# Performance work log

Hardware: AMD Instinct MI355X
Metric: run time of the kernel (lower is better)

## Reference

```python
import jax, jax.numpy as jnp
import numpy as np

NEG = -9e15  # matches torch's -9000000000000000.0 masking constant


def setup_inputs() -> dict:
    key = jax.random.key(0)
    kq, kk, kv, ka = jax.random.split(key, 4)
    B, H, N, d = 8, 8, 1024, 128
    queries = jax.random.normal(kq, (B, H, N, d), dtype=jnp.float32)
    keys = jax.random.normal(kk, (B, H, N, d), dtype=jnp.float32)
    values = jax.random.normal(kv, (B, H, N, d), dtype=jnp.float32)
    adj = jax.random.randint(ka, (N, N), 0, 2, dtype=jnp.int32)
    return {"queries": queries, "keys": keys, "values": values, "adj": adj}


def reference(queries, keys, values, adj):
    # scores: [B,H,N,N]; original divides by the constant 8 (not sqrt(dim))
    e = jnp.einsum("bhnd,bhmd->bhnm", queries, keys) / 8.0
    # adjacency mask [N,N] broadcasts over batch and heads
    att = jnp.where(adj > 0, e, jnp.asarray(NEG, e.dtype))
    att = jax.nn.softmax(att, axis=-1)
    # dropout is identity in eval mode
    h = jnp.einsum("bhnm,bhmd->bhnd", att, values)  # [B,H,N,d]
    B, H, N, d = h.shape
    # original uses .view (raw reshape), NOT a permute
    return jnp.reshape(h, (N, B, H, d))
```

## Files before the change

kernel.cpp:

```cpp
#include <hip/hip_runtime.h>
#include <hip/hip_bf16.h>


typedef __bf16 bf16x8 __attribute__((ext_vector_type(8)));
typedef float  f32x4  __attribute__((ext_vector_type(4)));
typedef unsigned int u32;
typedef unsigned long long u64;

#define NSEQ 1024
#define DH   128
#define BN   64
#define NKT  16
#define TILE_ELEMS (BN * DH)
#define C1 0.1803368801111244f
#define C2 11.5415603271110070f

__device__ __forceinline__ float f4get(const float4& v, int c) {
    return (c == 0) ? v.x : (c == 1) ? v.y : (c == 2) ? v.z : v.w;
}

__device__ __forceinline__ void gload_lds16(const void* g, void* l) {
    __builtin_amdgcn_global_load_lds(
        (const __attribute__((address_space(1))) u32*)g,
        (__attribute__((address_space(3))) u32*)l, 16, 0, 0);
}

__global__ __launch_bounds__(256)
void prepack_kernel(const float* __restrict__ K, const float* __restrict__ V,
                    __bf16* __restrict__ Kws, __bf16* __restrict__ Vws,
                    u64* __restrict__ adjp, const int* __restrict__ adj)
{
    const int tid = threadIdx.x;
    const int id  = blockIdx.x;

    if (id >= 1024) {
        const int r = (id - 1024) * 16 + (tid >> 4);
        const int c = tid & 15;
        const int* row = adj + (size_t)r * NSEQ + c;
        u64 w = 0;
        #pragma unroll
        for (int j = 0; j < 64; ++j)
            w |= (u64)(row[j * 16] > 0) << j;
        adjp[(size_t)r * 16 + c] = w;
        return;
    }

    const size_t gbase = (size_t)(id >> 4) * NSEQ * DH + (size_t)(id & 15) * BN * DH;
    __bf16* ko = Kws + (size_t)id * TILE_ELEMS;
    __bf16* vo = Vws + (size_t)id * TILE_ELEMS;

    {
        const int r  = tid >> 2;
        const int c0 = (tid & 3) * 4;
        #pragma unroll
        for (int cc = 0; cc < 4; ++cc) {
            const int c = c0 + cc;
            const float* src = K + gbase + (size_t)r * DH + c * 8;
            float4 a = *(const float4*)src;
            float4 b = *(const float4*)(src + 4);
            bf16x8 w;
            w[0]=(__bf16)a.x; w[1]=(__bf16)a.y; w[2]=(__bf16)a.z; w[3]=(__bf16)a.w;
            w[4]=(__bf16)b.x; w[5]=(__bf16)b.y; w[6]=(__bf16)b.z; w[7]=(__bf16)b.w;
            const int cs = (c & 8) | ((c ^ (r & 7)) & 7);
            *(bf16x8*)(ko + r * DH + cs * 8) = w;
        }
    }
    {
        const int vkvb = tid >> 5;
        const int vdb  = tid & 31;
        float4 vr[8];
        #pragma unroll
        for (int rr = 0; rr < 8; ++rr)
            vr[rr] = *(const float4*)(V + gbase + (size_t)(vkvb * 8 + rr) * DH + vdb * 4);
        #pragma unroll
        for (int c = 0; c < 4; ++c) {
            const int d = vdb * 4 + c;
            bf16x8 w;
            #pragma unroll
            for (int j = 0; j < 8; ++j) w[j] = (__bf16)f4get(vr[j], c);
            const int cs = vkvb ^ (d & 7);
            *(bf16x8*)(vo + d * BN + cs * 8) = w;
        }
    }
}

__global__ __launch_bounds__(512, 4)
void attn_fast(const float* __restrict__ Q, const __bf16* __restrict__ Kws,
               const __bf16* __restrict__ Vws, const u64* __restrict__ adjp,
               float* __restrict__ out)
{
    __shared__ __attribute__((aligned(16))) __bf16 Kt[2][TILE_ELEMS];
    __shared__ __attribute__((aligned(16))) __bf16 Vt[TILE_ELEMS];
    __shared__ __attribute__((aligned(16))) __bf16 Ps[128 * 72];

    const int tid  = threadIdx.x;
    const int wave = tid >> 6;
    const int lane = tid & 63;
    const int n16  = lane & 15;
    const int quad = lane >> 4;
    const int m7   = n16 & 7;

    const int id = blockIdx.x;
    const int bh = (id & 7) * 8 + ((id >> 3) & 7);
    const int q0 = (id >> 6) * 128;
    const size_t base  = (size_t)bh * NSEQ * DH;
    const size_t tile0 = (size_t)(bh * NKT) * TILE_ELEMS;
    const int qrb = q0 + wave * 16 + quad * 4;

    bf16x8 qf[4];
    #pragma unroll
    for (int ks = 0; ks < 4; ++ks) {
        const float* src = Q + base + (size_t)(q0 + wave * 16 + n16) * DH
                         + ks * 32 + quad * 8;
        float4 a = *(const float4*)src;
        float4 b = *(const float4*)(src + 4);
        bf16x8 w;
        w[0]=(__bf16)a.x; w[1]=(__bf16)a.y; w[2]=(__bf16)a.z; w[3]=(__bf16)a.w;
        w[4]=(__bf16)b.x; w[5]=(__bf16)b.y; w[6]=(__bf16)b.z; w[7]=(__bf16)b.w;
        qf[ks] = w;
    }

    u64 aw[4];
    #pragma unroll
    for (int i = 0; i < 4; ++i)
        aw[i] = adjp[(size_t)(qrb + i) * 16 + n16];

    f32x4 o[8];
    #pragma unroll
    for (int i = 0; i < 8; ++i) o[i] = (f32x4){0.f, 0.f, 0.f, 0.f};
    float lp[4] = {0.f, 0.f, 0.f, 0.f};

    #pragma unroll
    for (int j = 0; j < 2; ++j) {
        const int off = wave * 1024 + j * 512;
        gload_lds16(Kws + tile0 + off + lane * 8, &Kt[0][off]);
    }

    for (int kt = 0; kt < NKT; ++kt) {
        __builtin_amdgcn_sched_barrier(0);
        asm volatile("s_waitcnt vmcnt(0)" ::: "memory");
        __builtin_amdgcn_sched_barrier(0);
        __builtin_amdgcn_s_barrier();
        __builtin_amdgcn_sched_barrier(0);

        {
            const __bf16* vtile = Vws + tile0 + (size_t)kt * TILE_ELEMS;
            #pragma unroll
            for (int j = 0; j < 2; ++j) {
                const int off = wave * 1024 + j * 512;
                gload_lds16(vtile + off + lane * 8, &Vt[off]);
            }
        }
        __builtin_amdgcn_sched_barrier(0);

        {
            const int ktn = (kt + 1) & (NKT - 1);
            const __bf16* ktile = Kws + tile0 + (size_t)ktn * TILE_ELEMS;
            __bf16* kdst = &Kt[ktn & 1][0];
            #pragma unroll
            for (int j = 0; j < 2; ++j) {
                const int off = wave * 1024 + j * 512;
                gload_lds16(ktile + off + lane * 8, kdst + off);
            }
        }
        __builtin_amdgcn_sched_barrier(0);

        const __bf16* Kc = &Kt[kt & 1][0];
        float sc[4][4];
        __builtin_amdgcn_s_setprio(1);
        #pragma unroll
        for (int t = 0; t < 4; ++t) {
            f32x4 acc = (f32x4){0.f, 0.f, 0.f, 0.f};
            #pragma unroll
            for (int ks = 0; ks < 4; ++ks) {
                const int c  = ks * 4 + quad;
                const int cs = (c & 8) | ((c ^ m7) & 7);
                bf16x8 bfr = *(const bf16x8*)(Kc + (t * 16 + n16) * DH + cs * 8);
                acc = __builtin_amdgcn_mfma_f32_16x16x32_bf16(qf[ks], bfr, acc, 0, 0, 0);
            }
            #pragma unroll
            for (int i = 0; i < 4; ++i) sc[t][i] = acc[i];
        }
        __builtin_amdgcn_s_setprio(0);

        #pragma unroll
        for (int i = 0; i < 4; ++i) {
            const unsigned w4 = (unsigned)(aw[i] >> (kt * 4)) & 0xFu;
            const int prow = wave * 16 + quad * 4 + i;
            float rowsum = 0.f;
            #pragma unroll
            for (int t = 0; t < 4; ++t) {
                float p = exp2f(sc[t][i] * C1 - C2);
                p = (w4 & (1u << t)) ? p : 0.f;
                rowsum += p;
                Ps[prow * 72 + t * 16 + n16] = (__bf16)p;
            }
            lp[i] += rowsum;
        }

        __builtin_amdgcn_sched_barrier(0);
        asm volatile("s_waitcnt vmcnt(2) lgkmcnt(0)" ::: "memory");
        __builtin_amdgcn_sched_barrier(0);
        __builtin_amdgcn_s_barrier();
        __builtin_amdgcn_sched_barrier(0);

        __builtin_amdgcn_s_setprio(1);
        #pragma unroll
        for (int ks = 0; ks < 2; ++ks) {
            bf16x8 pf = *(const bf16x8*)(&Ps[(wave * 16 + n16) * 72 + ks * 32 + quad * 8]);
            #pragma unroll
            for (int nt = 0; nt < 8; ++nt) {
                const int d  = nt * 16 + n16;
                const int cs = (ks * 4 + quad) ^ m7;
                bf16x8 vf = *(const bf16x8*)(&Vt[d * BN + cs * 8]);
                o[nt] = __builtin_amdgcn_mfma_f32_16x16x32_bf16(pf, vf, o[nt], 0, 0, 0);
            }
        }
        __builtin_amdgcn_s_setprio(0);
    }

    float linv[4];
    #pragma unroll
    for (int i = 0; i < 4; ++i) {
        float ls = lp[i];
        ls += __shfl_xor(ls, 1);
        ls += __shfl_xor(ls, 2);
        ls += __shfl_xor(ls, 4);
        ls += __shfl_xor(ls, 8);
        linv[i] = 1.0f / fmaxf(ls, 1e-30f);
    }
    #pragma unroll
    for (int nt = 0; nt < 8; ++nt)
        #pragma unroll
        for (int i = 0; i < 4; ++i)
            out[base + (size_t)(qrb + i) * DH + nt * 16 + n16] = o[nt][i] * linv[i];
}

#define KS_STRIDE 136
#define VT_STRIDE 64
#define PS_STRIDE 72

__global__ __launch_bounds__(256, 4)
void attn_fallback(const float* __restrict__ Q, const float* __restrict__ K,
                   const float* __restrict__ V, const int* __restrict__ adj,
                   float* __restrict__ out)
{
    __shared__ __attribute__((aligned(16))) __bf16 KsP[BN * KS_STRIDE];
    __shared__ __attribute__((aligned(16))) __bf16 Vts[DH * VT_STRIDE];
    const int tid = threadIdx.x;
    const int wave = tid >> 6, lane = tid & 63, n16 = lane & 15, quad = lane >> 4;
    const int id = blockIdx.x;
    const int bh = (id & 7) * 8 + ((id >> 3) & 7);
    const int q0 = (id >> 6) * 64;
    const size_t base = (size_t)bh * NSEQ * DH;
    const int rp = tid >> 4, kcol = (tid & 15) * 8, db = tid & 31, kvb = tid >> 5;
    bf16x8 qf[4];
    #pragma unroll
    for (int ks = 0; ks < 4; ++ks) {
        const float* src = Q + base + (size_t)(q0 + wave * 16 + n16) * DH + ks * 32 + quad * 8;
        float4 a = *(const float4*)src; float4 b = *(const float4*)(src + 4);
        bf16x8 w;
        w[0]=(__bf16)a.x; w[1]=(__bf16)a.y; w[2]=(__bf16)a.z; w[3]=(__bf16)a.w;
        w[4]=(__bf16)b.x; w[5]=(__bf16)b.y; w[6]=(__bf16)b.z; w[7]=(__bf16)b.w;
        qf[ks] = w;
    }
    f32x4 o[8];
    #pragma unroll
    for (int i = 0; i < 8; ++i) o[i] = (f32x4){0.f, 0.f, 0.f, 0.f};
    float lp[4] = {0.f, 0.f, 0.f, 0.f};
    const int qrow = q0 + wave * 16 + quad * 4;
    for (int kt = 0; kt < NKT; ++kt) {
        const int kv0 = kt * BN;
        __syncthreads();
        #pragma unroll
        for (int it = 0; it < 4; ++it) {
            int row = 16 * it + rp;
            const float* src = K + base + (size_t)(kv0 + row) * DH + kcol;
            float4 a = *(const float4*)src; float4 b = *(const float4*)(src + 4);
            bf16x8 w;
            w[0]=(__bf16)a.x; w[1]=(__bf16)a.y; w[2]=(__bf16)a.z; w[3]=(__bf16)a.w;
            w[4]=(__bf16)b.x; w[5]=(__bf16)b.y; w[6]=(__bf16)b.z; w[7]=(__bf16)b.w;
            *(bf16x8*)(&KsP[row * KS_STRIDE + kcol]) = w;
        }
        {
            float4 vreg[8];
            #pragma unroll
            for (int rr = 0; rr < 8; ++rr)
                vreg[rr] = *(const float4*)(V + base + (size_t)(kv0 + kvb * 8 + rr) * DH + db * 4);
            #pragma unroll
            for (int c = 0; c < 4; ++c) {
                bf16x8 w;
                #pragma unroll
                for (int j = 0; j < 8; ++j) w[j] = (__bf16)f4get(vreg[j], c);
                int d = db * 4 + c, s = (d ^ (d >> 3)) & 7;
                *(bf16x8*)(&Vts[d * VT_STRIDE + ((kvb ^ s) << 3)]) = w;
            }
        }
        __syncthreads();
        int am[4][4];
        #pragma unroll
        for (int i = 0; i < 4; ++i)
            #pragma unroll
            for (int t = 0; t < 4; ++t)
                am[i][t] = adj[(size_t)(qrow + i) * NSEQ + kv0 + t * 16 + n16];
        float sc[4][4];
        #pragma unroll
        for (int t = 0; t < 4; ++t) {
            f32x4 acc = (f32x4){0.f, 0.f, 0.f, 0.f};
            #pragma unroll
            for (int ks = 0; ks < 4; ++ks) {
                bf16x8 bfr = *(const bf16x8*)(&KsP[(t * 16 + n16) * KS_STRIDE + ks * 32 + quad * 8]);
                acc = __builtin_amdgcn_mfma_f32_16x16x32_bf16(qf[ks], bfr, acc, 0, 0, 0);
            }
            #pragma unroll
            for (int i = 0; i < 4; ++i) sc[t][i] = acc[i];
        }
        __syncthreads();
        #pragma unroll
        for (int i = 0; i < 4; ++i) {
            const int prow = wave * 16 + quad * 4 + i;
            float rowsum = 0.f;
            #pragma unroll
            for (int t = 0; t < 4; ++t) {
                float p = exp2f(sc[t][i] * C1 - C2);
                p = (am[i][t] > 0) ? p : 0.f;
                rowsum += p;
                KsP[prow * PS_STRIDE + t * 16 + n16] = (__bf16)p;
            }
            lp[i] += rowsum;
        }
        #pragma unroll
        for (int ks = 0; ks < 2; ++ks) {
            bf16x8 pf = *(const bf16x8*)(&KsP[(wave * 16 + n16) * PS_STRIDE + ks * 32 + quad * 8]);
            #pragma unroll
            for (int nt = 0; nt < 8; ++nt) {
                int d = nt * 16 + n16, s = (d ^ (d >> 3)) & 7, kvbr = ks * 4 + quad;
                bf16x8 vf = *(const bf16x8*)(&Vts[d * VT_STRIDE + ((kvbr ^ s) << 3)]);
                o[nt] = __builtin_amdgcn_mfma_f32_16x16x32_bf16(pf, vf, o[nt], 0, 0, 0);
            }
        }
    }
    float linv[4];
    #pragma unroll
    for (int i = 0; i < 4; ++i) {
        float ls = lp[i];
        ls += __shfl_xor(ls, 1); ls += __shfl_xor(ls, 2);
        ls += __shfl_xor(ls, 4); ls += __shfl_xor(ls, 8);
        linv[i] = 1.0f / fmaxf(ls, 1e-30f);
    }
    #pragma unroll
    for (int nt = 0; nt < 8; ++nt)
        #pragma unroll
        for (int i = 0; i < 4; ++i)
            out[base + (size_t)(qrow + i) * DH + nt * 16 + n16] = o[nt][i] * linv[i];
}

extern "C" void kernel_launch(void* const* d_in, const int* in_sizes, int n_in,
                              void* d_out, int out_size, void* d_ws, size_t ws_size,
                              hipStream_t stream) {
    const float* Q   = (const float*)d_in[0];
    const float* K   = (const float*)d_in[1];
    const float* V   = (const float*)d_in[2];
    const int*   adj = (const int*)d_in[3];
    float* out = (float*)d_out;
    const size_t needKV  = (size_t)2 * 64 * NKT * TILE_ELEMS * sizeof(__bf16);
    const size_t needAdj = (size_t)NSEQ * 16 * sizeof(u64);
    if (ws_size >= needKV + needAdj) {
        __bf16* Kws = (__bf16*)d_ws;
        __bf16* Vws = Kws + (size_t)64 * NKT * TILE_ELEMS;
        u64* adjp = (u64*)(Vws + (size_t)64 * NKT * TILE_ELEMS);
        prepack_kernel<<<1088, 256, 0, stream>>>(K, V, Kws, Vws, adjp, adj);
        attn_fast<<<512, 512, 0, stream>>>(Q, Kws, Vws, adjp, out);
    } else {
        attn_fallback<<<1024, 256, 0, stream>>>(Q, K, V, adj, out);
    }
}
```

Baseline: 195.9 us.

## Switch attention to 32x32x16 MFMA tiles with 2x4 wave grid

Reorganizes the fast attention kernel so each wave computes a 32x32 score tile and a 32x64 output tile using 32x32x16 bf16 MFMA instead of 16x16x32, with waves arranged as 4 row groups by 2 column groups. The adjacency bitmask is repacked column-major into 32-bit words matching the new accumulator layout, and loaded per key tile inside the loop. Row sums are now split across column-group waves and combined via shared memory at the end. This aims at fewer LDS operand reads per MFMA and better matrix-core efficiency, at the cost of more accumulator registers and an extra cross-wave reduction.

```diff
diff --git a/kernel.cpp b/kernel.cpp
--- a/kernel.cpp
+++ b/kernel.cpp
@@ -4,8 +4,8 @@
 
 typedef __bf16 bf16x8 __attribute__((ext_vector_type(8)));
 typedef float  f32x4  __attribute__((ext_vector_type(4)));
+typedef float  f32x16 __attribute__((ext_vector_type(16)));
 typedef unsigned int u32;
-typedef unsigned long long u64;
 
 #define NSEQ 1024
 #define DH   128
@@ -28,20 +28,20 @@
 __global__ __launch_bounds__(256)
 void prepack_kernel(const float* __restrict__ K, const float* __restrict__ V,
                     __bf16* __restrict__ Kws, __bf16* __restrict__ Vws,
-                    u64* __restrict__ adjp, const int* __restrict__ adj)
+                    u32* __restrict__ adjc, const int* __restrict__ adj)
 {
     const int tid = threadIdx.x;
     const int id  = blockIdx.x;
 
     if (id >= 1024) {
-        const int r = (id - 1024) * 16 + (tid >> 4);
-        const int c = tid & 15;
-        const int* row = adj + (size_t)r * NSEQ + c;
-        u64 w = 0;
-        #pragma unroll
-        for (int j = 0; j < 64; ++j)
-            w |= (u64)(row[j * 16] > 0) << j;
-        adjp[(size_t)r * 16 + c] = w;
+        const int idx  = id - 1024;
+        const int rg32 = idx & 31;
+        const int kv   = (idx >> 5) * 256 + tid;
+        u32 w = 0;
+        #pragma unroll
+        for (int j = 0; j < 32; ++j)
+            w |= (u32)(adj[(size_t)(rg32 * 32 + j) * NSEQ + kv] > 0) << j;
+        adjc[(size_t)kv * 32 + rg32] = w;
         return;
     }
 
@@ -49,86 +49,96 @@
     __bf16* ko = Kws + (size_t)id * TILE_ELEMS;
     __bf16* vo = Vws + (size_t)id * TILE_ELEMS;
 
+    #pragma unroll
+    for (int p = 0; p < 4; ++p) {
+        const int r = p * 16 + (tid >> 4);
+        const int c = tid & 15;
+        const float* src = K + gbase + (size_t)r * DH + c * 8;
+        float4 a = *(const float4*)src;
+        float4 b = *(const float4*)(src + 4);
+        bf16x8 w;
+        w[0]=(__bf16)a.x; w[1]=(__bf16)a.y; w[2]=(__bf16)a.z; w[3]=(__bf16)a.w;
+        w[4]=(__bf16)b.x; w[5]=(__bf16)b.y; w[6]=(__bf16)b.z; w[7]=(__bf16)b.w;
+        const int cs = (c & 8) | ((c ^ (r & 7)) & 7);
+        *(bf16x8*)(ko + r * DH + cs * 8) = w;
+    }
     {
-        const int r  = tid >> 2;
-        const int c0 = (tid & 3) * 4;
-        #pragma unroll
-        for (int cc = 0; cc < 4; ++cc) {
-            const int c = c0 + cc;
-            const float* src = K + gbase + (size_t)r * DH + c * 8;
+        const int vkvb = tid >> 5;
+        const int vdb  = tid & 31;
+        float4 vr[8];
+        #pragma unroll
+        for (int rr = 0; rr < 8; ++rr)
+            vr[rr] = *(const float4*)(V + gbase + (size_t)(vkvb * 8 + rr) * DH + vdb * 4);
+        #pragma unroll
+        for (int c = 0; c < 4; ++c) {
+            const int d = vdb * 4 + c;
+            bf16x8 w;
+            #pragma unroll
+            for (int j = 0; j < 8; ++j) w[j] = (__bf16)f4get(vr[j], c);
+            const int cs = vkvb ^ (d & 7);
+            *(bf16x8*)(vo + d * BN + cs * 8) = w;
+        }
+    }
+}
+
+__global__ __launch_bounds__(512, 4)
+void attn_fast(const float* __restrict__ Q, const __bf16* __restrict__ Kws,
+               const __bf16* __restrict__ Vws, const u32* __restrict__ adjc,
+               float* __restrict__ out)
+{
+    __shared__ __attribute__((aligned(16))) __bf16 Kt[2][TILE_ELEMS];
+    __shared__ __attribute__((aligned(16))) __bf16 Vt[TILE_ELEMS];
+    __shared__ __attribute__((aligned(16))) __bf16 Ps[128 * BN];
+
+    const int tid  = threadIdx.x;
+    const int wave = tid >> 6;
+    const int lane = tid & 63;
+    const int l31  = lane & 31;
+    const int hi   = lane >> 5;
+    const int l7   = lane & 7;
+    const int rowg = wave >> 1;
+    const int colg = wave & 1;
+
+    const int id = blockIdx.x;
+    const int bh = (id & 7) * 8 + ((id >> 3) & 7);
+    const int q0 = (id >> 6) * 128;
+    const size_t base  = (size_t)bh * NSEQ * DH;
+    const size_t tile0 = (size_t)(bh * NKT) * TILE_ELEMS;
+
+    bf16x8 qf[8];
+    {
+        const float* qrowp = Q + base + (size_t)(q0 + rowg * 32 + l31) * DH + hi * 8;
+        #pragma unroll
+        for (int ks = 0; ks < 8; ++ks) {
+            const float* src = qrowp + ks * 16;
             float4 a = *(const float4*)src;
             float4 b = *(const float4*)(src + 4);
             bf16x8 w;
             w[0]=(__bf16)a.x; w[1]=(__bf16)a.y; w[2]=(__bf16)a.z; w[3]=(__bf16)a.w;
             w[4]=(__bf16)b.x; w[5]=(__bf16)b.y; w[6]=(__bf16)b.z; w[7]=(__bf16)b.w;
+            qf[ks] = w;
+        }
+    }
+
+    int kaddr[8];
+    {
+        const int r = colg * 32 + l31;
+        #pragma unroll
+        for (int ks = 0; ks < 8; ++ks) {
+            const int c  = ks * 2 + hi;
             const int cs = (c & 8) | ((c ^ (r & 7)) & 7);
-            *(bf16x8*)(ko + r * DH + cs * 8) = w;
-        }
-    }
-    {
-        const int vkvb = tid >> 5;
-        const int vdb  = tid & 31;
-        float4 vr[8];
-        #pragma unroll
-        for (int rr = 0; rr < 8; ++rr)
-            vr[rr] = *(const float4*)(V + gbase + (size_t)(vkvb * 8 + rr) * DH + vdb * 4);
-        #pragma unroll
-        for (int c = 0; c < 4; ++c) {
-            const int d = vdb * 4 + c;
-            bf16x8 w;
-            #pragma unroll
-            for (int j = 0; j < 8; ++j) w[j] = (__bf16)f4get(vr[j], c);
-            const int cs = vkvb ^ (d & 7);
-            *(bf16x8*)(vo + d * BN + cs * 8) = w;
-        }
-    }
-}
-
-__global__ __launch_bounds__(512, 4)
-void attn_fast(const float* __restrict__ Q, const __bf16* __restrict__ Kws,
-               const __bf16* __restrict__ Vws, const u64* __restrict__ adjp,
-               float* __restrict__ out)
-{
-    __shared__ __attribute__((aligned(16))) __bf16 Kt[2][TILE_ELEMS];
-    __shared__ __attribute__((aligned(16))) __bf16 Vt[TILE_ELEMS];
-    __shared__ __attribute__((aligned(16))) __bf16 Ps[128 * 72];
-
-    const int tid  = threadIdx.x;
-    const int wave = tid >> 6;
-    const int lane = tid & 63;
-    const int n16  = lane & 15;
-    const int quad = lane >> 4;
-    const int m7   = n16 & 7;
-
-    const int id = blockIdx.x;
-    const int bh = (id & 7) * 8 + ((id >> 3) & 7);
-    const int q0 = (id >> 6) * 128;
-    const size_t base  = (size_t)bh * NSEQ * DH;
-    const size_t tile0 = (size_t)(bh * NKT) * TILE_ELEMS;
-    const int qrb = q0 + wave * 16 + quad * 4;
-
-    bf16x8 qf[4];
-    #pragma unroll
-    for (int ks = 0; ks < 4; ++ks) {
-        const float* src = Q + base + (size_t)(q0 + wave * 16 + n16) * DH
-                         + ks * 32 + quad * 8;
-        float4 a = *(const float4*)src;
-        float4 b = *(const float4*)(src + 4);
-        bf16x8 w;
-        w[0]=(__bf16)a.x; w[1]=(__bf16)a.y; w[2]=(__bf16)a.z; w[3]=(__bf16)a.w;
-        w[4]=(__bf16)b.x; w[5]=(__bf16)b.y; w[6]=(__bf16)b.z; w[7]=(__bf16)b.w;
-        qf[ks] = w;
-    }
-
-    u64 aw[4];
-    #pragma unroll
-    for (int i = 0; i < 4; ++i)
-        aw[i] = adjp[(size_t)(qrb + i) * 16 + n16];
-
-    f32x4 o[8];
-    #pragma unroll
-    for (int i = 0; i < 8; ++i) o[i] = (f32x4){0.f, 0.f, 0.f, 0.f};
-    float lp[4] = {0.f, 0.f, 0.f, 0.f};
+            kaddr[ks] = (r * DH + cs * 8) * 2;
+        }
+    }
+
+    const size_t ab = (size_t)(colg * 32 + l31) * 32 + (q0 >> 5) + rowg;
+
+    f32x16 o0, o1;
+    #pragma unroll
+    for (int i = 0; i < 16; ++i) { o0[i] = 0.f; o1[i] = 0.f; }
+    float lp[16];
+    #pragma unroll
+    for (int i = 0; i < 16; ++i) lp[i] = 0.f;
 
     #pragma unroll
     for (int j = 0; j < 2; ++j) {
@@ -141,6 +151,9 @@
         asm volatile("s_waitcnt vmcnt(0)" ::: "memory");
         __builtin_amdgcn_sched_barrier(0);
         __builtin_amdgcn_s_barrier();
+        __builtin_amdgcn_sched_barrier(0);
+
+        const u32 am = adjc[ab + (size_t)kt * 2048];
         __builtin_amdgcn_sched_barrier(0);
 
         {
@@ -166,36 +179,30 @@
         __builtin_amdgcn_sched_barrier(0);
 
         const __bf16* Kc = &Kt[kt & 1][0];
-        float sc[4][4];
+        f32x16 s;
+        #pragma unroll
+        for (int i = 0; i < 16; ++i) s[i] = 0.f;
         __builtin_amdgcn_s_setprio(1);
         #pragma unroll
-        for (int t = 0; t < 4; ++t) {
-            f32x4 acc = (f32x4){0.f, 0.f, 0.f, 0.f};
-            #pragma unroll
-            for (int ks = 0; ks < 4; ++ks) {
-                const int c  = ks * 4 + quad;
-                const int cs = (c & 8) | ((c ^ m7) & 7);
-                bf16x8 bfr = *(const bf16x8*)(Kc + (t * 16 + n16) * DH + cs * 8);
-                acc = __builtin_amdgcn_mfma_f32_16x16x32_bf16(qf[ks], bfr, acc, 0, 0, 0);
-            }
-            #pragma unroll
-            for (int i = 0; i < 4; ++i) sc[t][i] = acc[i];
+        for (int ks = 0; ks < 8; ++ks) {
+            bf16x8 bfr = *(const bf16x8*)((const char*)Kc + kaddr[ks]);
+            s = __builtin_amdgcn_mfma_f32_32x32x16_bf16(qf[ks], bfr, s, 0, 0, 0);
         }
         __builtin_amdgcn_s_setprio(0);
 
-        #pragma unroll
-        for (int i = 0; i < 4; ++i) {
-            const unsigned w4 = (unsigned)(aw[i] >> (kt * 4)) & 0xFu;
-            const int prow = wave * 16 + quad * 4 + i;
-            float rowsum = 0.f;
-            #pragma unroll
-            for (int t = 0; t < 4; ++t) {
-                float p = exp2f(sc[t][i] * C1 - C2);
-                p = (w4 & (1u << t)) ? p : 0.f;
-                rowsum += p;
-                Ps[prow * 72 + t * 16 + n16] = (__bf16)p;
-            }
-            lp[i] += rowsum;
+        {
+            const u32 m2 = am >> (hi * 4);
+            const int chunk0 = colg * 4 + (l31 >> 3);
+            const int wbase  = (rowg * 32 + 4 * hi) * BN + l7;
+            #pragma unroll
+            for (int reg = 0; reg < 16; ++reg) {
+                const int rlo = (reg & 3) + 8 * (reg >> 2);
+                float p = exp2f(s[reg] * C1 - C2);
+                p = ((m2 >> rlo) & 1u) ? p : 0.f;
+                lp[reg] += p;
+                const int swc = chunk0 ^ ((reg & 3) | (hi << 2));
+                Ps[wbase + rlo * BN + swc * 8] = (__bf16)p;
+            }
         }
 
         __builtin_amdgcn_sched_barrier(0);
@@ -206,34 +213,46 @@
 
         __builtin_amdgcn_s_setprio(1);
         #pragma unroll
-        for (int ks = 0; ks < 2; ++ks) {
-            bf16x8 pf = *(const bf16x8*)(&Ps[(wave * 16 + n16) * 72 + ks * 32 + quad * 8]);
-            #pragma unroll
-            for (int nt = 0; nt < 8; ++nt) {
-                const int d  = nt * 16 + n16;
-                const int cs = (ks * 4 + quad) ^ m7;
-                bf16x8 vf = *(const bf16x8*)(&Vt[d * BN + cs * 8]);
-                o[nt] = __builtin_amdgcn_mfma_f32_16x16x32_bf16(pf, vf, o[nt], 0, 0, 0);
-            }
+        for (int kstep = 0; kstep < 4; ++kstep) {
+            const int chs = (kstep * 2 + hi) ^ l7;
+            bf16x8 pa = *(const bf16x8*)(&Ps[(rowg * 32 + l31) * BN + chs * 8]);
+            bf16x8 vf0 = *(const bf16x8*)(&Vt[(l31)      * BN + chs * 8 + colg * 64 * BN]);
+            o0 = __builtin_amdgcn_mfma_f32_32x32x16_bf16(pa, vf0, o0, 0, 0, 0);
+            bf16x8 vf1 = *(const bf16x8*)(&Vt[(32 + l31) * BN + chs * 8 + colg * 64 * BN]);
+            o1 = __builtin_amdgcn_mfma_f32_32x32x16_bf16(pa, vf1, o1, 0, 0, 0);
         }
         __builtin_amdgcn_s_setprio(0);
     }
 
-    float linv[4];
-    #pragma unroll
-    for (int i = 0; i < 4; ++i) {
-        float ls = lp[i];
+    #pragma unroll
+    for (int reg = 0; reg < 16; ++reg) {
+        float ls = lp[reg];
         ls += __shfl_xor(ls, 1);
         ls += __shfl_xor(ls, 2);
         ls += __shfl_xor(ls, 4);
         ls += __shfl_xor(ls, 8);
-        linv[i] = 1.0f / fmaxf(ls, 1e-30f);
-    }
-    #pragma unroll
-    for (int nt = 0; nt < 8; ++nt)
-        #pragma unroll
-        for (int i = 0; i < 4; ++i)
-            out[base + (size_t)(qrb + i) * DH + nt * 16 + n16] = o[nt][i] * linv[i];
+        ls += __shfl_xor(ls, 16);
+        lp[reg] = ls;
+    }
+    __syncthreads();
+    float* Ls = (float*)&Vt[0];
+    if (l31 == 0) {
+        #pragma unroll
+        for (int reg = 0; reg < 16; ++reg) {
+            const int row = rowg * 32 + (reg & 3) + 8 * (reg >> 2) + 4 * hi;
+            Ls[colg * 128 + row] = lp[reg];
+        }
+    }
+    __syncthreads();
+    #pragma unroll
+    for (int reg = 0; reg < 16; ++reg) {
+        const int row = rowg * 32 + (reg & 3) + 8 * (reg >> 2) + 4 * hi;
+        const float ls = Ls[row] + Ls[128 + row];
+        const float linv = 1.0f / fmaxf(ls, 1e-30f);
+        float* orow = out + base + (size_t)(q0 + row) * DH + colg * 64 + l31;
+        orow[0]  = o0[reg] * linv;
+        orow[32] = o1[reg] * linv;
+    }
 }
 
 #define KS_STRIDE 136
@@ -364,13 +383,13 @@
     const int*   adj = (const int*)d_in[3];
     float* out = (float*)d_out;
     const size_t needKV  = (size_t)2 * 64 * NKT * TILE_ELEMS * sizeof(__bf16);
-    const size_t needAdj = (size_t)NSEQ * 16 * sizeof(u64);
+    const size_t needAdj = (size_t)NSEQ * 32 * sizeof(u32);
     if (ws_size >= needKV + needAdj) {
         __bf16* Kws = (__bf16*)d_ws;
         __bf16* Vws = Kws + (size_t)64 * NKT * TILE_ELEMS;
-        u64* adjp = (u64*)(Vws + (size_t)64 * NKT * TILE_ELEMS);
-        prepack_kernel<<<1088, 256, 0, stream>>>(K, V, Kws, Vws, adjp, adj);
-        attn_fast<<<512, 512, 0, stream>>>(Q, Kws, Vws, adjp, out);
+        u32* adjc = (u32*)(Vws + (size_t)64 * NKT * TILE_ELEMS);
+        prepack_kernel<<<1152, 256, 0, stream>>>(K, V, Kws, Vws, adjc, adj);
+        attn_fast<<<512, 512, 0, stream>>>(Q, Kws, Vws, adjc, out);
     } else {
         attn_fallback<<<1024, 256, 0, stream>>>(Q, K, V, adj, out);
     }
```

Result: slower. 250.1 us (+27.7%).
